# Performance work log

Measured on AMD Instinct MI355X. Metric: run time of the kernel, lower is better.

The kernel has to match this reference:

```python
import jax, jax.numpy as jnp
import numpy as np

# Direction order matches shifted_c_map[:, :, i] = shift(c_map, Directable[TL_table[i]])
# TL_table = [lower_right, down, lower_left, right, left, upper_right, up, upper_left]
DIRS = [(1, 1), (0, 1), (-1, 1), (1, 0), (-1, 0), (1, -1), (0, -1), (-1, -1)]


def _shift(img, dx, dy):
    """Zero-filled pixel shift of [B,C,H,W]; equivalent to the bmm against the
    one-hot translation matrices in the torch code (dx=1 -> shift right, dy=1 -> shift down)."""
    H, W = img.shape[-2], img.shape[-1]
    if dx == 1:
        img = jnp.pad(img, ((0, 0), (0, 0), (0, 0), (1, 0)))[..., :W]
    elif dx == -1:
        img = jnp.pad(img, ((0, 0), (0, 0), (0, 0), (0, 1)))[..., 1:]
    if dy == 1:
        img = jnp.pad(img, ((0, 0), (0, 0), (1, 0), (0, 0)))[..., :H, :]
    elif dy == -1:
        img = jnp.pad(img, ((0, 0), (0, 0), (0, 1), (0, 0)))[..., 1:, :]
    return img


def setup_inputs() -> dict:
    key = jax.random.key(0)
    k1, k2, k3 = jax.random.split(key, 3)
    B, C, H, W = 16, 2, 512, 512
    c_map = jax.random.normal(k1, (B, C, H, W), dtype=jnp.float32)
    target = jax.random.randint(k2, (B, H, W), 0, 2, dtype=jnp.int64)
    con_target = jax.random.randint(k3, (B, 8, H, W), 0, 2).astype(jnp.float32)
    return {"c_map": c_map, "target": target, "con_target": con_target}


def reference(c_map, target, con_target):
    # Bilater_voting: all 8 copies along dim 2 are identical to c_map, so
    # shifted_c_map[:, :, i] = shift(c_map, DIRS[i]).
    shifted = jnp.stack([_shift(c_map, dx, dy) for dx, dy in DIRS], axis=2)  # [B,C,8,H,W]
    vote_out = c_map[:, :, None, :, :] * shifted                              # bimap [B,C,8,H,W]

    # CrossEntropyLoss(c_map, target)
    logp = jax.nn.log_softmax(c_map, axis=1)                                  # [B,C,H,W]
    ce_l = -jnp.mean(jnp.take_along_axis(logp, target[:, None, :, :], axis=1))

    # edge_loss(bimap.squeeze(1)=bimap since C>1, con_target)
    p = jax.nn.softmax(vote_out, axis=1)                                      # softmax over class dim
    sum_conn = 2.0 * con_target                                               # concat-dup then sum over dim 1
    edge = ((sum_conn < 8.0) & (sum_conn > 0.0)).astype(c_map.dtype)          # [B,8,H,W]
    pred_mask_min = jnp.min(p, axis=1) * edge                                 # [B,8,H,W]
    # F.binary_cross_entropy(p, 0) = mean(-log(1-p)), log clamped at -100 like torch
    minloss = jnp.mean(-jnp.clip(jnp.log1p(-pred_mask_min), -100.0, None))

    return 0.2 * minloss + 0.8 * ce_l
```

## Files before the change

### kernel.cpp

```cpp
#include <hip/hip_runtime.h>

#define BB 16
#define HH 512
#define WW 512
#define NPIX ((double)(BB * HH * WW))
#define NBLOCKS_MAX 2048


__global__ __launch_bounds__(256) void bicon_main(
    const float* __restrict__ cmap,
    const int*   __restrict__ target,
    const float* __restrict__ con,
    double* __restrict__ partials,
    int total_quads)
{
    constexpr int dxs[8] = {1, 0, -1, 1, -1, 1, 0, -1};
    constexpr int dys[8] = {1, 1,  1, 0,  0, -1, -1, -1};
    const int W4 = WW / 4;

    float acc_ce = 0.0f;
    float acc_min = 0.0f;

    const int stride = gridDim.x * blockDim.x;
    for (int idx = blockIdx.x * blockDim.x + threadIdx.x; idx < total_quads; idx += stride) {
        const int w4 = (idx & (W4 - 1)) * 4;
        const int h  = (idx >> 7) & (HH - 1);
        const int b  = idx >> 16;

        const float* __restrict__ c0p = cmap + (size_t)(b * 2 + 0) * HH * WW;
        const float* __restrict__ c1p = cmap + (size_t)(b * 2 + 1) * HH * WW;
        const int row = h * WW + w4;

        const float4 c0v = *(const float4*)(c0p + row);
        const float4 c1v = *(const float4*)(c1p + row);
        const int4   tgv = *(const int4*)(target + (size_t)b * HH * WW + row);

        const float cc0[4] = {c0v.x, c0v.y, c0v.z, c0v.w};
        const float cc1[4] = {c1v.x, c1v.y, c1v.z, c1v.w};
        const int   tt[4]  = {tgv.x, tgv.y, tgv.z, tgv.w};

        #pragma unroll
        for (int j = 0; j < 4; ++j) {
            const float m   = fmaxf(cc0[j], cc1[j]);
            const float lse = m + logf(expf(cc0[j] - m) + expf(cc1[j] - m));
            const float ct  = (tt[j] == 0) ? cc0[j] : cc1[j];
            acc_ce += (lse - ct);
        }

        #pragma unroll
        for (int i = 0; i < 8; ++i) {
            const int dx = dxs[i];
            const int dy = dys[i];
            const int hh = h - dy;
            const bool rowok = (hh >= 0) && (hh < HH);
            const float4 cv = *(const float4*)(con + (size_t)(b * 8 + i) * HH * WW + row);
            const float cts[4] = {cv.x, cv.y, cv.z, cv.w};

            #pragma unroll
            for (int j = 0; j < 4; ++j) {
                const int ww = w4 + j - dx;
                const bool ok = rowok && (ww >= 0) && (ww < WW);
                const int noff = hh * WW + ww;
                const float n0 = ok ? c0p[noff] : 0.0f;
                const float n1 = ok ? c1p[noff] : 0.0f;
                const float d  = cc0[j] * n0 - cc1[j] * n1;
                const float term = log1pf(expf(-fabsf(d)));
                const float t2 = 2.0f * cts[j];
                const float edge = (t2 < 8.0f && t2 > 0.0f) ? 1.0f : 0.0f;
                acc_min += edge * term;
            }
        }
    }

    double contrib = (double)acc_ce * (0.8 / NPIX)
                   + (double)acc_min * (0.2 / (8.0 * NPIX));

    #pragma unroll
    for (int off = 32; off > 0; off >>= 1)
        contrib += __shfl_down(contrib, off);

    __shared__ double sm[4];
    const int lane = threadIdx.x & 63;
    const int wid  = threadIdx.x >> 6;
    if (lane == 0) sm[wid] = contrib;
    __syncthreads();
    if (threadIdx.x == 0)
        partials[blockIdx.x] = sm[0] + sm[1] + sm[2] + sm[3];
}

__global__ __launch_bounds__(256) void bicon_finalize(
    const double* __restrict__ partials, int n, float* __restrict__ out)
{
    double s = 0.0;
    for (int i = threadIdx.x; i < n; i += blockDim.x) s += partials[i];
    #pragma unroll
    for (int off = 32; off > 0; off >>= 1)
        s += __shfl_down(s, off);

    __shared__ double sm[4];
    const int lane = threadIdx.x & 63;
    const int wid  = threadIdx.x >> 6;
    if (lane == 0) sm[wid] = s;
    __syncthreads();
    if (threadIdx.x == 0)
        out[0] = (float)(sm[0] + sm[1] + sm[2] + sm[3]);
}

extern "C" void kernel_launch(void* const* d_in, const int* in_sizes, int n_in,
                              void* d_out, int out_size, void* d_ws, size_t ws_size,
                              hipStream_t stream) {
    const float* cmap   = (const float*)d_in[0];
    const int*   target = (const int*)d_in[1];
    const float* con    = (const float*)d_in[2];
    float* out = (float*)d_out;
    double* partials = (double*)d_ws;

    int nblocks = NBLOCKS_MAX;
    const size_t cap = ws_size / sizeof(double);
    if ((size_t)nblocks > cap) nblocks = (int)cap;
    if (nblocks < 1) nblocks = 1;

    const int total_quads = BB * HH * (WW / 4);

    bicon_main<<<nblocks, 256, 0, stream>>>(cmap, target, con, partials, total_quads);
    bicon_finalize<<<1, 256, 0, stream>>>(partials, nblocks, out);
}
```

Baseline: 266.2 us.

## Cache 3x6 neighborhood in registers and use hardware exp2/log2 for softplus

Loads the 3-row by 6-column neighborhood of both channels once per quad with vector loads, replacing 64 scalar gathers per quad with a few float4 and edge loads. Rewrites the cross-entropy as max(lin,0)+softplus(-|dl|) and evaluates all softplus terms with the native exp2/log2 intrinsics in base 2, applying ln2 scaling once at the end. This targets redundant memory traffic and the cost of libm exp/log/log1p, at the price of slightly lower precision from the hardware approximations and 1+x instead of log1p.

```diff
diff --git a/kernel.cpp b/kernel.cpp
--- a/kernel.cpp
+++ b/kernel.cpp
@@ -3,8 +3,15 @@
 #define BB 16
 #define HH 512
 #define WW 512
+#define HWSZ (HH * WW)
 #define NPIX ((double)(BB * HH * WW))
 #define NBLOCKS_MAX 2048
+
+#define L2E 1.4426950408889634f
+#define LN2 0.6931471805599453
+
+__device__ __forceinline__ float hw_exp2(float x) { return __builtin_amdgcn_exp2f(x); }
+__device__ __forceinline__ float hw_log2(float x) { return __builtin_amdgcn_logf(x); }
 
 
 __global__ __launch_bounds__(256) void bicon_main(
@@ -16,64 +23,87 @@
 {
     constexpr int dxs[8] = {1, 0, -1, 1, -1, 1, 0, -1};
     constexpr int dys[8] = {1, 1,  1, 0,  0, -1, -1, -1};
-    const int W4 = WW / 4;
 
-    float acc_ce = 0.0f;
-    float acc_min = 0.0f;
+    float acc_min_l2 = 0.0f;
+    float acc_ce_l2  = 0.0f;
+    float acc_ce_lin = 0.0f;
 
     const int stride = gridDim.x * blockDim.x;
     for (int idx = blockIdx.x * blockDim.x + threadIdx.x; idx < total_quads; idx += stride) {
-        const int w4 = (idx & (W4 - 1)) * 4;
-        const int h  = (idx >> 7) & (HH - 1);
+        const int w4 = (idx & 127) * 4;
+        const int h  = (idx >> 7) & 511;
         const int b  = idx >> 16;
 
-        const float* __restrict__ c0p = cmap + (size_t)(b * 2 + 0) * HH * WW;
-        const float* __restrict__ c1p = cmap + (size_t)(b * 2 + 1) * HH * WW;
+        const float* __restrict__ c0p = cmap + (size_t)(b * 2) * HWSZ;
+        const float* __restrict__ c1p = c0p + HWSZ;
         const int row = h * WW + w4;
 
         const float4 c0v = *(const float4*)(c0p + row);
         const float4 c1v = *(const float4*)(c1p + row);
-        const int4   tgv = *(const int4*)(target + (size_t)b * HH * WW + row);
+        const int4   tgv = *(const int4*)(target + (size_t)b * HWSZ + row);
 
         const float cc0[4] = {c0v.x, c0v.y, c0v.z, c0v.w};
         const float cc1[4] = {c1v.x, c1v.y, c1v.z, c1v.w};
         const int   tt[4]  = {tgv.x, tgv.y, tgv.z, tgv.w};
 
+        const bool lok = (w4 > 0);
+        const bool rok = (w4 + 4 < WW);
+
+        float n0[3][6], n1[3][6];
+
+        {
+            const float* p0 = c0p + row;
+            const float* p1 = c1p + row;
+            n0[1][1] = c0v.x; n0[1][2] = c0v.y; n0[1][3] = c0v.z; n0[1][4] = c0v.w;
+            n1[1][1] = c1v.x; n1[1][2] = c1v.y; n1[1][3] = c1v.z; n1[1][4] = c1v.w;
+            n0[1][0] = lok ? p0[-1] : 0.0f;  n0[1][5] = rok ? p0[4] : 0.0f;
+            n1[1][0] = lok ? p1[-1] : 0.0f;  n1[1][5] = rok ? p1[4] : 0.0f;
+        }
+        #pragma unroll
+        for (int r = 0; r < 3; r += 2) {
+            const int hh = h + r - 1;
+            const bool rowok = (hh >= 0) && (hh < HH);
+            const float* p0 = c0p + hh * WW + w4;
+            const float* p1 = c1p + hh * WW + w4;
+            if (rowok) {
+                const float4 v0 = *(const float4*)p0;
+                const float4 v1 = *(const float4*)p1;
+                n0[r][1] = v0.x; n0[r][2] = v0.y; n0[r][3] = v0.z; n0[r][4] = v0.w;
+                n1[r][1] = v1.x; n1[r][2] = v1.y; n1[r][3] = v1.z; n1[r][4] = v1.w;
+                n0[r][0] = lok ? p0[-1] : 0.0f;  n0[r][5] = rok ? p0[4] : 0.0f;
+                n1[r][0] = lok ? p1[-1] : 0.0f;  n1[r][5] = rok ? p1[4] : 0.0f;
+            } else {
+                #pragma unroll
+                for (int c = 0; c < 6; ++c) { n0[r][c] = 0.0f; n1[r][c] = 0.0f; }
+            }
+        }
+
         #pragma unroll
         for (int j = 0; j < 4; ++j) {
-            const float m   = fmaxf(cc0[j], cc1[j]);
-            const float lse = m + logf(expf(cc0[j] - m) + expf(cc1[j] - m));
-            const float ct  = (tt[j] == 0) ? cc0[j] : cc1[j];
-            acc_ce += (lse - ct);
+            const float dl = cc0[j] - cc1[j];
+            acc_ce_l2 += hw_log2(1.0f + hw_exp2(-fabsf(dl) * L2E));
+            const float lin = (tt[j] == 0) ? -dl : dl;
+            acc_ce_lin += fmaxf(lin, 0.0f);
         }
 
         #pragma unroll
         for (int i = 0; i < 8; ++i) {
-            const int dx = dxs[i];
-            const int dy = dys[i];
-            const int hh = h - dy;
-            const bool rowok = (hh >= 0) && (hh < HH);
-            const float4 cv = *(const float4*)(con + (size_t)(b * 8 + i) * HH * WW + row);
+            const float4 cv = *(const float4*)(con + (size_t)(b * 8 + i) * HWSZ + row);
             const float cts[4] = {cv.x, cv.y, cv.z, cv.w};
-
+            const int rr = 1 - dys[i];
             #pragma unroll
             for (int j = 0; j < 4; ++j) {
-                const int ww = w4 + j - dx;
-                const bool ok = rowok && (ww >= 0) && (ww < WW);
-                const int noff = hh * WW + ww;
-                const float n0 = ok ? c0p[noff] : 0.0f;
-                const float n1 = ok ? c1p[noff] : 0.0f;
-                const float d  = cc0[j] * n0 - cc1[j] * n1;
-                const float term = log1pf(expf(-fabsf(d)));
-                const float t2 = 2.0f * cts[j];
-                const float edge = (t2 < 8.0f && t2 > 0.0f) ? 1.0f : 0.0f;
-                acc_min += edge * term;
+                const int cidx = j - dxs[i] + 1;
+                const float d = fmaf(cc0[j], n0[rr][cidx], -(cc1[j] * n1[rr][cidx]));
+                const float t2   = 2.0f * cts[j];
+                const float term = hw_log2(1.0f + hw_exp2(-fabsf(d) * L2E));
+                acc_min_l2 += (t2 > 0.0f && t2 < 8.0f) ? term : 0.0f;
             }
         }
     }
 
-    double contrib = (double)acc_ce * (0.8 / NPIX)
-                   + (double)acc_min * (0.2 / (8.0 * NPIX));
+    double contrib = (0.8 / NPIX) * ((double)acc_ce_lin + LN2 * (double)acc_ce_l2)
+                   + (0.2 * LN2 / (8.0 * NPIX)) * (double)acc_min_l2;
 
     #pragma unroll
     for (int off = 32; off > 0; off >>= 1)
```

Result: faster. 226.9 us (-14.8%).
